# Performance work log

Hardware: AMD Instinct MI355X
Metric: run time of the kernel (lower is better)

Reference implementation:

```python
import jax, jax.numpy as jnp
import numpy as np

E = 1024   # embd_size
H = 16     # heads_num
DH = E // H
DFF = 4 * E
B, T = 2, 2048


def layer_norm(x, g, b, eps=1e-5):
    mu = jnp.mean(x, axis=-1, keepdims=True)
    var = jnp.var(x, axis=-1, keepdims=True)
    return (x - mu) * jax.lax.rsqrt(var + eps) * g + b


def setup_inputs() -> dict:
    key = jax.random.key(0)
    ks = jax.random.split(key, 12)
    s = 0.02
    return {
        "x": jax.random.normal(ks[0], (B, T, E), dtype=jnp.float32),
        "Wq": jax.random.normal(ks[1], (E, E), dtype=jnp.float32) * s,
        "Wk": jax.random.normal(ks[2], (E, E), dtype=jnp.float32) * s,
        "Wv": jax.random.normal(ks[3], (E, E), dtype=jnp.float32) * s,
        "Wo": jax.random.normal(ks[4], (E, E), dtype=jnp.float32) * s,
        "bo": jnp.zeros((E,), dtype=jnp.float32),
        "W1": jax.random.normal(ks[5], (E, DFF), dtype=jnp.float32) * s,
        "b1": jnp.zeros((DFF,), dtype=jnp.float32),
        "W2": jax.random.normal(ks[6], (DFF, E), dtype=jnp.float32) * s,
        "b2": jnp.zeros((E,), dtype=jnp.float32),
        "g1": jnp.ones((E,), dtype=jnp.float32),
        "be1": jnp.zeros((E,), dtype=jnp.float32),
        "g2": jnp.ones((E,), dtype=jnp.float32),
        "be2": jnp.zeros((E,), dtype=jnp.float32),
    }


def reference(x, Wq, Wk, Wv, Wo, bo, W1, b1, W2, b2, g1, be1, g2, be2):
    Bx, Tx, C = x.shape
    # --- self-attention sublayer ---
    h = layer_norm(x, g1, be1)
    # per-head projections; heads concatenated along output dim == stacked weights
    q = (h @ Wq).reshape(Bx, Tx, H, DH)  # [B,T,H,Dh]
    k = (h @ Wk).reshape(Bx, Tx, H, DH)
    v = (h @ Wv).reshape(Bx, Tx, H, DH)
    # NOTE: original scales by full embd_size**-0.5 (C = x.shape[-1]), not head_size
    scale = C ** (-0.5)
    scores = jnp.einsum("bqhd,bkhd->bhqk", q, k) * scale  # [B,H,T,T]
    mask = jnp.tril(jnp.ones((Tx, Tx), dtype=bool))
    scores = jnp.where(mask, scores, -jnp.inf)
    attn = jax.nn.softmax(scores, axis=-1)
    o = jnp.einsum("bhqk,bkhd->bqhd", attn, v).reshape(Bx, Tx, C)
    sa = o @ Wo + bo
    x = x + sa
    # --- feed-forward sublayer ---
    h2 = layer_norm(x, g2, be2)
    ff = jax.nn.relu(h2 @ W1 + b1) @ W2 + b2
    return x + ff
```

## Files before the change

### kernel.cpp

```cpp
#include <hip/hip_runtime.h>
#include <hip/hip_bf16.h>
#include <math.h>

#define Bn 2
#define Tn 2048
#define En 1024
#define Hn 16
#define DFFn 4096
#define Mn (Bn*Tn)
#define QKVLD 3072

typedef __hip_bfloat16 bf16;
typedef unsigned short u16;
typedef unsigned int u32;
typedef __attribute__((ext_vector_type(8))) short short8;
typedef __attribute__((ext_vector_type(4))) float f32x4;

typedef __attribute__((address_space(1))) const void cg_void;
typedef __attribute__((address_space(3))) void lds_void;

#define QSC 0.0450842200278f

#define HBAR() asm volatile("s_waitcnt lgkmcnt(0)\n\ts_barrier" ::: "memory")

__device__ __forceinline__ u16 f2bf(float f) {
    bf16 h = __float2bfloat16(f);
    u16 u; __builtin_memcpy(&u, &h, 2); return u;
}
__device__ __forceinline__ float bf2f(u16 u) {
    u32 x = ((u32)u) << 16; float f; __builtin_memcpy(&f, &x, 4); return f;
}

__global__ __launch_bounds__(256)
void transpose_w4(const float* __restrict__ s0, const float* __restrict__ s1,
                  const float* __restrict__ s2, const float* __restrict__ s3,
                  u16* __restrict__ d0, u16* __restrict__ d1,
                  u16* __restrict__ d2, u16* __restrict__ d3) {
    const float* src = (blockIdx.z == 0) ? s0 : (blockIdx.z == 1) ? s1
                     : (blockIdx.z == 2) ? s2 : s3;
    u16* dst = (blockIdx.z == 0) ? d0 : (blockIdx.z == 1) ? d1
             : (blockIdx.z == 2) ? d2 : d3;
    __shared__ float t[64][65];
    const int r0 = blockIdx.y * 64, c0 = blockIdx.x * 64;
    const int tr = threadIdx.x >> 6, tc = threadIdx.x & 63;
#pragma unroll
    for (int i = 0; i < 16; i++)
        t[tr + i * 4][tc] = src[(size_t)(r0 + tr + i * 4) * 1024 + c0 + tc];
    __syncthreads();
#pragma unroll
    for (int i = 0; i < 16; i++)
        dst[(size_t)(c0 + tr + i * 4) * 1024 + r0 + tc] = f2bf(t[tc][tr + i * 4]);
}

__global__ __launch_bounds__(256)
void transpose_w(const float* __restrict__ src, u16* __restrict__ dst,
                 int R, int C) {
    __shared__ float t[64][65];
    const int r0 = blockIdx.y * 64, c0 = blockIdx.x * 64;
    const int tr = threadIdx.x >> 6, tc = threadIdx.x & 63;
#pragma unroll
    for (int i = 0; i < 16; i++)
        t[tr + i * 4][tc] = src[(size_t)(r0 + tr + i * 4) * C + c0 + tc];
    __syncthreads();
#pragma unroll
    for (int i = 0; i < 16; i++)
        dst[(size_t)(c0 + tr + i * 4) * R + r0 + tc] = f2bf(t[tc][tr + i * 4]);
}

__global__ __launch_bounds__(256)
void vcopy_t(const u16* __restrict__ QKV, u16* __restrict__ Vg) {
    const int bh = blockIdx.z;
    const int t0 = blockIdx.y * 64;
    __shared__ u16 t[64][65];
    const int tr = threadIdx.x >> 6, tc = threadIdx.x & 63;
    const u16* src = QKV + (size_t)(bh >> 4) * 2048 * QKVLD + 2048 + (bh & 15) * 64;
#pragma unroll
    for (int i = 0; i < 16; i++)
        t[tr + i * 4][tc] = src[(size_t)(t0 + tr + i * 4) * QKVLD + tc];
    __syncthreads();
    u16* dst = Vg + (size_t)bh * 64 * 2048;
#pragma unroll
    for (int i = 0; i < 16; i++)
        dst[(size_t)(tr + i * 4) * 2048 + t0 + tc] = t[tc][tr + i * 4];
}

template<typename AT>
__global__ __launch_bounds__(256)
void ln_kernel(const AT* __restrict__ x, const float* __restrict__ g,
               const float* __restrict__ b, u16* __restrict__ out) {
    const int row = blockIdx.x;
    const int tid = threadIdx.x;
    const AT* xp = x + (size_t)row * En;
    float v[4];
    float s = 0.f, sq = 0.f;
#pragma unroll
    for (int i = 0; i < 4; i++) {
        if constexpr (sizeof(AT) == 2) v[i] = bf2f(xp[tid + i * 256]);
        else                           v[i] = (float)xp[tid + i * 256];
        s += v[i];
        sq += v[i] * v[i];
    }
    __shared__ float rs[256], rq[256];
    rs[tid] = s; rq[tid] = sq;
    __syncthreads();
    for (int st = 128; st > 0; st >>= 1) {
        if (tid < st) { rs[tid] += rs[tid + st]; rq[tid] += rq[tid + st]; }
        __syncthreads();
    }
    const float mu  = rs[0] * (1.0f / En);
    const float var = rq[0] * (1.0f / En) - mu * mu;
    const float inv = rsqrtf(var + 1e-5f);
#pragma unroll
    for (int i = 0; i < 4; i++) {
        const int c = tid + i * 256;
        out[(size_t)row * En + c] = f2bf((v[i] - mu) * inv * g[c] + b[c]);
    }
}

template<int TM, int HAS_BIAS, int RELU, int RES, int OUT_F32, int SCQ>
__global__ __launch_bounds__(256)
void gemm_bt(const u16* __restrict__ A, int ldA,
             const u16* __restrict__ Wt, int ldW,
             const float* __restrict__ bias, const void* __restrict__ res,
             void* __restrict__ Cout, int ldC, int Kd) {
    constexpr int IF = TM / 32;
    __shared__ __align__(16) u16 As[TM * 32];
    __shared__ __align__(16) u16 Bs[128 * 32];
    const int tid  = threadIdx.x;
    const int lane = tid & 63, wv = tid >> 6;
    const int quad = lane >> 4, l16 = lane & 15;
    const int m0 = blockIdx.y * TM, n0 = blockIdx.x * 128;
    const int rw = (wv >> 1) * (TM / 2), cw = (wv & 1) * 64;
    const int lr  = lane >> 2;
    const int gsw = ((lane & 3) ^ ((lane >> 3) & 3)) * 8;
    const int psw = (quad ^ ((l16 >> 1) & 3)) * 8;

    f32x4 acc[IF][4] = {};

    for (int kt = 0; kt < Kd; kt += 32) {
        __syncthreads();
#pragma unroll
        for (int t = 0; t < TM / 64; t++) {
            const int row = wv * (TM / 4) + t * 16;
            __builtin_amdgcn_global_load_lds(
                (cg_void*)(const void*)&A[(size_t)(m0 + row + lr) * ldA + kt + gsw],
                (lds_void*)(void*)&As[row * 32], 16, 0, 0);
        }
#pragma unroll
        for (int t = 0; t < 2; t++) {
            const int row = wv * 32 + t * 16;
            __builtin_amdgcn_global_load_lds(
                (cg_void*)(const void*)&Wt[(size_t)(n0 + row + lr) * ldW + kt + gsw],
                (lds_void*)(void*)&Bs[row * 32], 16, 0, 0);
        }
        __syncthreads();

        short8 af[IF], bfr[4];
#pragma unroll
        for (int i = 0; i < IF; i++)
            af[i] = *(const short8*)&As[(rw + i * 16 + l16) * 32 + psw];
#pragma unroll
        for (int j = 0; j < 4; j++)
            bfr[j] = *(const short8*)&Bs[(cw + j * 16 + l16) * 32 + psw];
#pragma unroll
        for (int i = 0; i < IF; i++)
#pragma unroll
            for (int j = 0; j < 4; j++)
                acc[i][j] = __builtin_amdgcn_mfma_f32_16x16x32_bf16(
                    af[i], bfr[j], acc[i][j], 0, 0, 0);
    }

    const float qscale = (SCQ && n0 < 1024) ? QSC : 1.0f;
#pragma unroll
    for (int i = 0; i < IF; i++) {
#pragma unroll
        for (int r = 0; r < 4; r++) {
            const int gm = m0 + rw + i * 16 + quad * 4 + r;
#pragma unroll
            for (int j = 0; j < 4; j++) {
                const int gn = n0 + cw + j * 16 + l16;
                float c = acc[i][j][r];
                if (HAS_BIAS) c += bias[gn];
                if (RELU) c = fmaxf(c, 0.f);
                if (RES == 1) c += ((const float*)res)[(size_t)gm * ldC + gn];
                if (RES == 2) c += bf2f(((const u16*)res)[(size_t)gm * ldC + gn]);
                if (SCQ) c *= qscale;
                if (OUT_F32) ((float*)Cout)[(size_t)gm * ldC + gn] = c;
                else         ((u16*)Cout)[(size_t)gm * ldC + gn] = f2bf(c);
            }
        }
    }
}

__global__ __launch_bounds__(256)
void flash_pass1(const u16* __restrict__ QKV, const u16* __restrict__ Vg,
                 u16* __restrict__ Op0, u16* __restrict__ Op1qkv,
                 float* __restrict__ stats) {
    const int pr = blockIdx.x >> 1, half = blockIdx.x & 1;
    const int hh = blockIdx.y, bb = blockIdx.z;
    const int tid  = threadIdx.x;
    const int lane = tid & 63, wv = tid >> 6;
    const int quad = lane >> 4, l16 = lane & 15;

    __shared__ __align__(16) u16 Ks[2][64 * 64];
    __shared__ __align__(16) u16 Vt[2][64 * 64];
    __shared__ __align__(16) u16 Ps[4][16 * 64];

    const size_t rowbase = (size_t)(bb * Tn) * QKVLD;
    const u16* Vgh = Vg + (size_t)(bb * Hn + hh) * 64 * 2048;

    const int sr = tid >> 2;
    const int p0 = (tid & 3) | ((sr & 1) << 2);
    const int p1 = p0 ^ 4;
    const int g0 = p0 ^ (sr & 7), g1 = p1 ^ (sr & 7);
    const int lsw = l16 & 7;

    uint4 kA, kB, vA, vB;
    auto prefetch = [&](int kt) {
        const size_t kb = rowbase + (size_t)(kt * 64 + sr) * QKVLD + 1024 + hh * 64;
        kA = *(const uint4*)&QKV[kb + g0 * 8];
        kB = *(const uint4*)&QKV[kb + g1 * 8];
        const size_t vb = (size_t)sr * 2048 + kt * 64;
        vA = *(const uint4*)&Vgh[vb + g0 * 8];
        vB = *(const uint4*)&Vgh[vb + g1 * 8];
    };
    auto writebuf = [&](int buf) {
        *(uint4*)&Ks[buf][sr * 64 + p0 * 8] = kA;
        *(uint4*)&Ks[buf][sr * 64 + p1 * 8] = kB;
        *(uint4*)&Vt[buf][sr * 64 + p0 * 8] = vA;
        *(uint4*)&Vt[buf][sr * 64 + p1 * 8] = vB;
    };

    for (int qsel = 0; qsel < 2; qsel++) {
        const int qt = qsel ? (31 - pr) : pr;
        const int nk = (qt >= half) ? ((qt - half) >> 1) + 1 : 0;
        const int qrow = qt * 64 + wv * 16 + l16;
        const int grow = bb * Tn + qrow;

        f32x4 ot[4] = {};
        float m2 = -INFINITY, lrow = 0.f;

        HBAR();
        if (nk > 0) {
            const u16* qp = QKV + rowbase + (size_t)qrow * QKVLD + hh * 64;
            short8 qf[2];
            qf[0] = *(const short8*)&qp[quad * 8];
            qf[1] = *(const short8*)&qp[32 + quad * 8];

            prefetch(half);
            writebuf(0);
            if (nk > 1) prefetch(half + 2);
            HBAR();

            const bool hasdiag = ((qt ^ half) & 1) == 0;
            for (int f = 0; f < nk; f++) {
                const int cur = f & 1;

                f32x4 st[4] = {};
#pragma unroll
                for (int ks = 0; ks < 2; ks++)
#pragma unroll
                    for (int i = 0; i < 4; i++) {
                        short8 kf = *(const short8*)&Ks[cur][(i * 16 + l16) * 64 +
                                     (((ks * 4 + quad) ^ lsw) * 8)];
                        st[i] = __builtin_amdgcn_mfma_f32_16x16x32_bf16(
                            kf, qf[ks], st[i], 0, 0, 0);
                    }

                float tmax = -INFINITY;
                if (hasdiag && f == nk - 1) {
                    const int qloc = wv * 16 + l16;
#pragma unroll
                    for (int i = 0; i < 4; i++)
#pragma unroll
                        for (int r = 0; r < 4; r++) {
                            float s = st[i][r];
                            if (i * 16 + quad * 4 + r > qloc) s = -INFINITY;
                            st[i][r] = s;
                            tmax = fmaxf(tmax, s);
                        }
                } else {
#pragma unroll
                    for (int i = 0; i < 4; i++)
#pragma unroll
                        for (int r = 0; r < 4; r++)
                            tmax = fmaxf(tmax, st[i][r]);
                }
                tmax = fmaxf(tmax, __shfl_xor(tmax, 16));
                tmax = fmaxf(tmax, __shfl_xor(tmax, 32));

                const float mnew = fmaxf(m2, tmax);
                const float alpha = exp2f(m2 - mnew);
                m2 = mnew;
                float psum = 0.f;
#pragma unroll
                for (int i = 0; i < 4; i++)
#pragma unroll
                    for (int r = 0; r < 4; r++) {
                        const float e = exp2f(st[i][r] - mnew);
                        st[i][r] = e;
                        psum += e;
                    }
                psum += __shfl_xor(psum, 16);
                psum += __shfl_xor(psum, 32);
                lrow = lrow * alpha + psum;
#pragma unroll
                for (int i = 0; i < 4; i++) ot[i] *= alpha;

#pragma unroll
                for (int i = 0; i < 4; i++) {
                    uint2 w;
                    w.x = (u32)f2bf(st[i][0]) | ((u32)f2bf(st[i][1]) << 16);
                    w.y = (u32)f2bf(st[i][2]) | ((u32)f2bf(st[i][3]) << 16);
                    const int g = (i * 2 + (quad >> 1)) ^ lsw;
                    *(uint2*)&Ps[wv][l16 * 64 + g * 8 + (quad & 1) * 4] = w;
                }
                asm volatile("s_waitcnt lgkmcnt(0)" ::: "memory");

#pragma unroll
                for (int ks = 0; ks < 2; ks++) {
                    short8 pf = *(const short8*)&Ps[wv][l16 * 64 +
                                 (((ks * 4 + quad) ^ lsw) * 8)];
#pragma unroll
                    for (int i = 0; i < 4; i++) {
                        short8 vf = *(const short8*)&Vt[cur][(i * 16 + l16) * 64 +
                                     (((ks * 4 + quad) ^ lsw) * 8)];
                        ot[i] = __builtin_amdgcn_mfma_f32_16x16x32_bf16(
                            vf, pf, ot[i], 0, 0, 0);
                    }
                }

                if (f + 1 < nk) {
                    writebuf(cur ^ 1);
                    if (f + 2 < nk) prefetch(half + 2 * (f + 2));
                    HBAR();
                }
            }
        }

        if (half == 0) {
            u16* op = Op0 + (size_t)grow * 1024 + hh * 64;
#pragma unroll
            for (int i = 0; i < 4; i++) {
                ushort4 o4;
                o4.x = f2bf(ot[i][0]); o4.y = f2bf(ot[i][1]);
                o4.z = f2bf(ot[i][2]); o4.w = f2bf(ot[i][3]);
                *(ushort4*)&op[i * 16 + quad * 4] = o4;
            }
        } else {
            u16* op = Op1qkv + (size_t)grow * QKVLD + 2048 + hh * 64;
#pragma unroll
            for (int i = 0; i < 4; i++) {
                ushort4 o4;
                o4.x = f2bf(ot[i][0]); o4.y = f2bf(ot[i][1]);
                o4.z = f2bf(ot[i][2]); o4.w = f2bf(ot[i][3]);
                *(ushort4*)&op[i * 16 + quad * 4] = o4;
            }
        }
        if (quad == 0) {
            stats[((size_t)(half * 2 + 0) * 4096 + grow) * 16 + hh] = m2;
            stats[((size_t)(half * 2 + 1) * 4096 + grow) * 16 + hh] = lrow;
        }
    }
}

__global__ __launch_bounds__(256)
void flash_merge(u16* __restrict__ QKV, const u16* __restrict__ Op0,
                 const float* __restrict__ stats) {
    const int row = blockIdx.x;
    const int tid = threadIdx.x;
    const int col = tid * 4;
    const int hh = col >> 6;
    const float m0 = stats[((size_t)0 * 4096 + row) * 16 + hh];
    const float l0 = stats[((size_t)1 * 4096 + row) * 16 + hh];
    const float m1 = stats[((size_t)2 * 4096 + row) * 16 + hh];
    const float l1 = stats[((size_t)3 * 4096 + row) * 16 + hh];
    const float m  = fmaxf(m0, m1);
    const float w0 = exp2f(m0 - m), w1 = exp2f(m1 - m);
    const float inv = 1.0f / (w0 * l0 + w1 * l1);
    ushort4 a = *(const ushort4*)&Op0[(size_t)row * 1024 + col];
    ushort4 b = *(const ushort4*)&QKV[(size_t)row * QKVLD + 2048 + col];
    ushort4 o;
    o.x = f2bf((w0 * bf2f(a.x) + w1 * bf2f(b.x)) * inv);
    o.y = f2bf((w0 * bf2f(a.y) + w1 * bf2f(b.y)) * inv);
    o.z = f2bf((w0 * bf2f(a.z) + w1 * bf2f(b.z)) * inv);
    o.w = f2bf((w0 * bf2f(a.w) + w1 * bf2f(b.w)) * inv);
    *(ushort4*)&QKV[(size_t)row * QKVLD + col] = o;
}

extern "C" void kernel_launch(void* const* d_in, const int* in_sizes, int n_in,
                              void* d_out, int out_size, void* d_ws, size_t ws_size,
                              hipStream_t stream) {
    const float* x   = (const float*)d_in[0];
    const float* Wq  = (const float*)d_in[1];
    const float* Wk  = (const float*)d_in[2];
    const float* Wv  = (const float*)d_in[3];
    const float* Wo  = (const float*)d_in[4];
    const float* bo  = (const float*)d_in[5];
    const float* W1  = (const float*)d_in[6];
    const float* b1  = (const float*)d_in[7];
    const float* W2  = (const float*)d_in[8];
    const float* b2  = (const float*)d_in[9];
    const float* g1  = (const float*)d_in[10];
    const float* be1 = (const float*)d_in[11];
    const float* g2  = (const float*)d_in[12];
    const float* be2 = (const float*)d_in[13];

    char* wsb = (char*)d_ws;
    u16*   QKV = (u16*)wsb;
    u16*   F1  = (u16*)wsb;
    u16*   W2T = (u16*)(wsb + 16u * 1024 * 1024);
    u16*   Op0 = (u16*)(wsb + 24u * 1024 * 1024);
    u16*   X1b = Op0;
    u16*   Vg  = (u16*)(wsb + 32u * 1024 * 1024);
    u16*   h     = (u16*)d_out;
    u16*   WT    = (u16*)((char*)d_out + 8u * 1024 * 1024);
    u16*   WqkvT = WT;
    u16*   WoT   = WT + 3u * 1024 * 1024;
    float* stats = (float*)WT;
    u16*   W1T   = WT;

    transpose_w4<<<dim3(16, 16, 4), 256, 0, stream>>>(
        Wq, Wk, Wv, Wo,
        WqkvT, WqkvT + 1024u * 1024, WqkvT + 2048u * 1024, WoT);

    ln_kernel<float><<<Mn, 256, 0, stream>>>(x, g1, be1, h);

    gemm_bt<128, 0, 0, 0, 0, 1><<<dim3(24, 32), 256, 0, stream>>>(
        h, En, WqkvT, En, nullptr, nullptr, QKV, QKVLD, En);

    vcopy_t<<<dim3(1, 32, 32), 256, 0, stream>>>(QKV, Vg);

    flash_pass1<<<dim3(32, Hn, Bn), 256, 0, stream>>>(QKV, Vg, Op0, QKV, stats);

    flash_merge<<<Mn, 256, 0, stream>>>(QKV, Op0, stats);

    gemm_bt<64, 1, 0, 1, 0, 0><<<dim3(8, 64), 256, 0, stream>>>(
        QKV, QKVLD, WoT, En, bo, x, X1b, En, En);

    transpose_w<<<dim3(64, 16), 256, 0, stream>>>(W1, W1T, 1024, 4096);
    transpose_w<<<dim3(16, 64), 256, 0, stream>>>(W2, W2T, 4096, 1024);

    ln_kernel<u16><<<Mn, 256, 0, stream>>>(X1b, g2, be2, h);

    gemm_bt<128, 1, 1, 0, 0, 0><<<dim3(16, 32), 256, 0, stream>>>(
        h, En, W1T, En, b1, nullptr, F1, 2048, En);
    gemm_bt<64, 0, 0, 2, 0, 0><<<dim3(8, 64), 256, 0, stream>>>(
        F1, 2048, W2T, DFFn, nullptr, X1b, X1b, En, 2048);
    gemm_bt<128, 1, 1, 0, 0, 0><<<dim3(16, 32), 256, 0, stream>>>(
        h, En, W1T + 2048u * 1024, En, b1 + 2048, nullptr, F1, 2048, En);
    gemm_bt<64, 1, 0, 2, 1, 0><<<dim3(8, 64), 256, 0, stream>>>(
        F1, 2048, W2T + 2048, DFFn, b2, X1b, (float*)d_out, En, 2048);
}
```

Before: 392.1 us.

## Merge split FFN GEMMs into single full-width launches using two scratch buffers

```diff
diff --git a/kernel.cpp b/kernel.cpp
--- a/kernel.cpp
+++ b/kernel.cpp
@@ -117,12 +117,14 @@
     }
 }
 
-template<int TM, int HAS_BIAS, int RELU, int RES, int OUT_F32, int SCQ>
-__global__ __launch_bounds__(256)
-void gemm_bt(const u16* __restrict__ A, int ldA,
+template<int TM, int HAS_BIAS, int RELU, int RES, int OUT_F32, int SCQ,
+         int SPLITC, int SPLITA>
+__global__ __launch_bounds__(256)
+void gemm_bt(const u16* __restrict__ A, const u16* __restrict__ A2, int ldA,
              const u16* __restrict__ Wt, int ldW,
              const float* __restrict__ bias, const void* __restrict__ res,
-             void* __restrict__ Cout, int ldC, int Kd) {
+             void* __restrict__ Cout, void* __restrict__ Cout2,
+             int ldC, int Kd) {
     constexpr int IF = TM / 32;
     __shared__ __align__(16) u16 As[TM * 32];
     __shared__ __align__(16) u16 Bs[128 * 32];
@@ -138,12 +140,14 @@
     f32x4 acc[IF][4] = {};
 
     for (int kt = 0; kt < Kd; kt += 32) {
+        const u16* Ap = (SPLITA && kt >= 2048) ? A2 : A;
+        const int  kk = SPLITA ? (kt & 2047) : kt;
         __syncthreads();
 #pragma unroll
         for (int t = 0; t < TM / 64; t++) {
             const int row = wv * (TM / 4) + t * 16;
             __builtin_amdgcn_global_load_lds(
-                (cg_void*)(const void*)&A[(size_t)(m0 + row + lr) * ldA + kt + gsw],
+                (cg_void*)(const void*)&Ap[(size_t)(m0 + row + lr) * ldA + kk + gsw],
                 (lds_void*)(void*)&As[row * 32], 16, 0, 0);
         }
 #pragma unroll
@@ -171,6 +175,7 @@
     }
 
     const float qscale = (SCQ && n0 < 1024) ? QSC : 1.0f;
+    void* Cp = (SPLITC && n0 >= 2048) ? Cout2 : Cout;
 #pragma unroll
     for (int i = 0; i < IF; i++) {
 #pragma unroll
@@ -179,14 +184,15 @@
 #pragma unroll
             for (int j = 0; j < 4; j++) {
                 const int gn = n0 + cw + j * 16 + l16;
+                const int cn = SPLITC ? (gn & 2047) : gn;
                 float c = acc[i][j][r];
                 if (HAS_BIAS) c += bias[gn];
                 if (RELU) c = fmaxf(c, 0.f);
-                if (RES == 1) c += ((const float*)res)[(size_t)gm * ldC + gn];
-                if (RES == 2) c += bf2f(((const u16*)res)[(size_t)gm * ldC + gn]);
+                if (RES == 1) c += ((const float*)res)[(size_t)gm * ldC + cn];
+                if (RES == 2) c += bf2f(((const u16*)res)[(size_t)gm * ldC + cn]);
                 if (SCQ) c *= qscale;
-                if (OUT_F32) ((float*)Cout)[(size_t)gm * ldC + gn] = c;
-                else         ((u16*)Cout)[(size_t)gm * ldC + gn] = f2bf(c);
+                if (OUT_F32) ((float*)Cp)[(size_t)gm * ldC + cn] = c;
+                else         ((u16*)Cp)[(size_t)gm * ldC + cn] = f2bf(c);
             }
         }
     }
@@ -338,24 +344,14 @@
             }
         }
 
-        if (half == 0) {
-            u16* op = Op0 + (size_t)grow * 1024 + hh * 64;
-#pragma unroll
-            for (int i = 0; i < 4; i++) {
-                ushort4 o4;
-                o4.x = f2bf(ot[i][0]); o4.y = f2bf(ot[i][1]);
-                o4.z = f2bf(ot[i][2]); o4.w = f2bf(ot[i][3]);
-                *(ushort4*)&op[i * 16 + quad * 4] = o4;
-            }
-        } else {
-            u16* op = Op1qkv + (size_t)grow * QKVLD + 2048 + hh * 64;
-#pragma unroll
-            for (int i = 0; i < 4; i++) {
-                ushort4 o4;
-                o4.x = f2bf(ot[i][0]); o4.y = f2bf(ot[i][1]);
-                o4.z = f2bf(ot[i][2]); o4.w = f2bf(ot[i][3]);
-                *(ushort4*)&op[i * 16 + quad * 4] = o4;
-            }
+        u16* op = (half == 0) ? (Op0 + (size_t)grow * 1024 + hh * 64)
+                              : (Op1qkv + (size_t)grow * QKVLD + 2048 + hh * 64);
+#pragma unroll
+        for (int i = 0; i < 4; i++) {
+            ushort4 o4;
+            o4.x = f2bf(ot[i][0]); o4.y = f2bf(ot[i][1]);
+            o4.z = f2bf(ot[i][2]); o4.w = f2bf(ot[i][3]);
+            *(ushort4*)&op[i * 16 + quad * 4] = o4;
         }
         if (quad == 0) {
             stats[((size_t)(half * 2 + 0) * 4096 + grow) * 16 + hh] = m2;
@@ -408,11 +404,12 @@
 
     char* wsb = (char*)d_ws;
     u16*   QKV = (u16*)wsb;
-    u16*   F1  = (u16*)wsb;
+    u16*   F1a = (u16*)wsb;
     u16*   W2T = (u16*)(wsb + 16u * 1024 * 1024);
     u16*   Op0 = (u16*)(wsb + 24u * 1024 * 1024);
     u16*   X1b = Op0;
     u16*   Vg  = (u16*)(wsb + 32u * 1024 * 1024);
+    u16*   F1b = Vg;
     u16*   h     = (u16*)d_out;
     u16*   WT    = (u16*)((char*)d_out + 8u * 1024 * 1024);
     u16*   WqkvT = WT;
@@ -426,8 +423,8 @@
 
     ln_kernel<float><<<Mn, 256, 0, stream>>>(x, g1, be1, h);
 
-    gemm_bt<128, 0, 0, 0, 0, 1><<<dim3(24, 32), 256, 0, stream>>>(
-        h, En, WqkvT, En, nullptr, nullptr, QKV, QKVLD, En);
+    gemm_bt<128, 0, 0, 0, 0, 1, 0, 0><<<dim3(24, 32), 256, 0, stream>>>(
+        h, nullptr, En, WqkvT, En, nullptr, nullptr, QKV, nullptr, QKVLD, En);
 
     vcopy_t<<<dim3(1, 32, 32), 256, 0, stream>>>(QKV, Vg);
 
@@ -435,20 +432,17 @@
 
     flash_merge<<<Mn, 256, 0, stream>>>(QKV, Op0, stats);
 
-    gemm_bt<64, 1, 0, 1, 0, 0><<<dim3(8, 64), 256, 0, stream>>>(
-        QKV, QKVLD, WoT, En, bo, x, X1b, En, En);
+    gemm_bt<64, 1, 0, 1, 0, 0, 0, 0><<<dim3(8, 64), 256, 0, stream>>>(
+        QKV, nullptr, QKVLD, WoT, En, bo, x, X1b, nullptr, En, En);
 
     transpose_w<<<dim3(64, 16), 256, 0, stream>>>(W1, W1T, 1024, 4096);
     transpose_w<<<dim3(16, 64), 256, 0, stream>>>(W2, W2T, 4096, 1024);
 
     ln_kernel<u16><<<Mn, 256, 0, stream>>>(X1b, g2, be2, h);
 
-    gemm_bt<128, 1, 1, 0, 0, 0><<<dim3(16, 32), 256, 0, stream>>>(
-        h, En, W1T, En, b1, nullptr, F1, 2048, En);
-    gemm_bt<64, 0, 0, 2, 0, 0><<<dim3(8, 64), 256, 0, stream>>>(
-        F1, 2048, W2T, DFFn, nullptr, X1b, X1b, En, 2048);
-    gemm_bt<128, 1, 1, 0, 0, 0><<<dim3(16, 32), 256, 0, stream>>>(
-        h, En, W1T + 2048u * 1024, En, b1 + 2048, nullptr, F1, 2048, En);
-    gemm_bt<64, 1, 0, 2, 1, 0><<<dim3(8, 64), 256, 0, stream>>>(
-        F1, 2048, W2T + 2048, DFFn, b2, X1b, (float*)d_out, En, 2048);
-}
+    gemm_bt<128, 1, 1, 0, 0, 0, 1, 0><<<dim3(32, 32), 256, 0, stream>>>(
+        h, nullptr, En, W1T, En, b1, nullptr, F1a, F1b, 2048, En);
+
+    gemm_bt<64, 1, 0, 2, 1, 0, 0, 1><<<dim3(8, 64), 256, 0, stream>>>(
+        F1a, F1b, 2048, W2T, DFFn, b2, X1b, (float*)d_out, nullptr, En, DFFn);
+}
```

Measured after the change: 386.1 us. Within noise of the previous version (-1.5%).
